# Optimization experiments

Measured on AMD Instinct MI355X. Metric: run time of the kernel, lower is better.

## Reference

```python
import jax, jax.numpy as jnp
import numpy as np

N_R, N_V, D, E_RR, L, G = 50000, 2000, 128, 800000, 3, 32


def setup_inputs() -> dict:
    key = jax.random.key(0)
    ks = jax.random.split(key, 10)
    x_real = jax.random.normal(ks[0], (N_R, D), dtype=jnp.float32)
    x_virtual = jax.random.normal(ks[1], (N_V, D), dtype=jnp.float32)
    # params: [num_layers, 3 relations (r_to_r, r_to_v, v_to_r), D, D]
    W_root = jax.random.normal(ks[2], (L, 3, D, D), dtype=jnp.float32) * 0.05
    W_nbr = jax.random.normal(ks[3], (L, 3, D, D), dtype=jnp.float32) * 0.05
    bias = jax.random.normal(ks[4], (L, 3, D), dtype=jnp.float32) * 0.05
    edge_rr = jax.random.randint(ks[5], (2, E_RR), 0, N_R)
    # one virtual-node edge per real node (hierarchical virtual nodes)
    src_rv = jnp.arange(N_R)
    dst_rv = jax.random.randint(ks[6], (N_R,), 0, N_V)
    edge_rv = jnp.stack([src_rv, dst_rv])          # real -> virtual
    edge_vr = jnp.stack([dst_rv, src_rv])          # virtual -> real
    batch_real = jnp.sort(jax.random.randint(ks[7], (N_R,), 0, G))
    return {
        "x_real": x_real, "x_virtual": x_virtual,
        "W_root": W_root, "W_nbr": W_nbr, "bias": bias,
        "edge_rr": edge_rr, "edge_rv": edge_rv, "edge_vr": edge_vr,
        "batch_real": batch_real,
    }


def _graph_conv(x_src, x_dst, src, dst, Wr, Wn, b, n_dst):
    # PyG GraphConv-style: root transform + sum-aggregated neighbor messages
    msg = jax.ops.segment_sum(x_src[src] @ Wn, dst, num_segments=n_dst)
    return x_dst @ Wr + msg + b


def _forward(x_real, x_virtual, W_root, W_nbr, bias, edge_rr, edge_rv, edge_vr, batch_real):
    x_r, x_v = x_real, x_virtual
    n_r, n_v = x_r.shape[0], x_v.shape[0]
    for l in range(W_root.shape[0]):
        # HeteroConv with aggr='sum': sum relation outputs per destination type
        c_rr = _graph_conv(x_r, x_r, edge_rr[0], edge_rr[1], W_root[l, 0], W_nbr[l, 0], bias[l, 0], n_r)
        c_vr = _graph_conv(x_v, x_r, edge_vr[0], edge_vr[1], W_root[l, 2], W_nbr[l, 2], bias[l, 2], n_r)
        c_rv = _graph_conv(x_r, x_v, edge_rv[0], edge_rv[1], W_root[l, 1], W_nbr[l, 1], bias[l, 1], n_v)
        # activation + dropout (eval mode -> identity)
        x_r = jax.nn.relu(c_rr + c_vr)
        x_v = jax.nn.relu(c_rv)
    # mean readout over real nodes per graph
    counts = jax.ops.segment_sum(jnp.ones((n_r,), x_r.dtype), batch_real, num_segments=G)
    graph_emb = jax.ops.segment_sum(x_r, batch_real, num_segments=G) / jnp.maximum(counts, 1.0)[:, None]
    return x_r, graph_emb


def reference(x_real, x_virtual, W_root, W_nbr, bias, edge_rr, edge_rv, edge_vr, batch_real):
    node_embedding, graph_embedding = _forward(
        x_real, x_virtual, W_root, W_nbr, bias, edge_rr, edge_rv, edge_vr, batch_real)
    return node_embedding, graph_embedding
```

## Files before the change

kernel.cpp:

```cpp
#include <hip/hip_runtime.h>
#include <hip/hip_bf16.h>

#define N_R   50000
#define N_V   2000
#define DIM   128
#define E_RR  800000
#define NLAY  3
#define NGR   32
#define RCHUNK 16

#define BUKD  128
#define NBUK  391
#define CHKE  2048
#define NCHK  391

typedef __attribute__((ext_vector_type(8))) short bf16x8;
typedef __attribute__((ext_vector_type(4))) float f32x4;
typedef __attribute__((ext_vector_type(2))) float f32x2;
typedef __attribute__((ext_vector_type(8))) unsigned char u8x8;

__device__ __forceinline__ ushort f2bf(float f) {
    unsigned u = __builtin_bit_cast(unsigned, f);
    unsigned r = (u + 0x7fffu + ((u >> 16) & 1u)) >> 16;
    return (ushort)r;
}
__device__ __forceinline__ float bf2f(ushort h) {
    unsigned u = ((unsigned)h) << 16;
    return __builtin_bit_cast(float, u);
}
__device__ __forceinline__ int lbound(const int* __restrict__ a, int n, int key) {
    int lo = 0, hi = n;
    while (lo < hi) { int mid = (lo + hi) >> 1; if (a[mid] < key) lo = mid + 1; else hi = mid; }
    return lo;
}

__device__ __forceinline__ void acc_u8row(
    unsigned w0, unsigned w1, float s,
    f32x2& a01, f32x2& a23, f32x2& a45, f32x2& a67)
{
    f32x2 sc = {s, s};
    a01 += sc * (f32x2){(float)(w0 & 0xffu), (float)((w0 >> 8) & 0xffu)};
    a23 += sc * (f32x2){(float)((w0 >> 16) & 0xffu), (float)(w0 >> 24)};
    a45 += sc * (f32x2){(float)(w1 & 0xffu), (float)((w1 >> 8) & 0xffu)};
    a67 += sc * (f32x2){(float)((w1 >> 16) & 0xffu), (float)(w1 >> 24)};
}

__global__ __launch_bounds__(256) void hist_kernel(
    const int* __restrict__ dst, int n, int* __restrict__ cnt)
{
    int i = blockIdx.x * 256 + threadIdx.x;
    if (i < n) atomicAdd(&cnt[dst[i]], 1);
}

__global__ __launch_bounds__(256) void scan_single_kernel(
    const int* __restrict__ cnt, int n, int nedges,
    int* __restrict__ rowptr, int* __restrict__ cursor)
{
    __shared__ int lds[256];
    __shared__ int carry;
    int t = threadIdx.x;
    if (t == 0) carry = 0;
    __syncthreads();
    for (int base = 0; base < n; base += 256) {
        int i = base + t;
        int v = (i < n) ? cnt[i] : 0;
        lds[t] = v;
        __syncthreads();
        #pragma unroll
        for (int off = 1; off < 256; off <<= 1) {
            int u = (t >= off) ? lds[t - off] : 0;
            __syncthreads();
            lds[t] += u;
            __syncthreads();
        }
        int excl = carry + lds[t] - v;
        if (i < n) {
            rowptr[i] = excl;
            if (cursor) cursor[i] = excl;
        }
        __syncthreads();
        if (t == 255) carry += lds[255];
        __syncthreads();
    }
    if (t == 0) rowptr[n] = nedges;
}

__global__ __launch_bounds__(256) void fill_kernel(
    const int* __restrict__ src, const int* __restrict__ dst, int n,
    int* __restrict__ cursor, int* __restrict__ col)
{
    int i = blockIdx.x * 256 + threadIdx.x;
    if (i < n) {
        int p = atomicAdd(&cursor[dst[i]], 1);
        col[p] = src[i];
    }
}

__global__ __launch_bounds__(256) void bkt_count_kernel(
    const int* __restrict__ dst, unsigned short* __restrict__ cnt2d)
{
    __shared__ int h[NBUK];
    int t = threadIdx.x, c = blockIdx.x;
    for (int i = t; i < NBUK; i += 256) h[i] = 0;
    __syncthreads();
    int e0 = c * CHKE, e1 = min(e0 + CHKE, E_RR);
    for (int e = e0 + t; e < e1; e += 256) atomicAdd(&h[dst[e] >> 7], 1);
    __syncthreads();
    for (int i = t; i < NBUK; i += 256)
        cnt2d[(size_t)c * NBUK + i] = (unsigned short)h[i];
}

__global__ __launch_bounds__(64) void bkt_prefix_kernel(
    const unsigned short* __restrict__ cnt2d,
    unsigned short* __restrict__ rel2d, int* __restrict__ tot)
{
    int b = blockIdx.x, lane = threadIdx.x;
    int base = 0;
    for (int c0 = 0; c0 < NCHK; c0 += 64) {
        int c = c0 + lane;
        int v = (c < NCHK) ? (int)cnt2d[(size_t)c * NBUK + b] : 0;
        int s = v;
        #pragma unroll
        for (int off = 1; off < 64; off <<= 1) {
            int u = __shfl_up(s, off);
            if (lane >= off) s += u;
        }
        if (c < NCHK) rel2d[(size_t)c * NBUK + b] = (unsigned short)(base + s - v);
        base += __shfl(s, 63);
    }
    if (lane == 0) tot[b] = base;
}

__global__ __launch_bounds__(256) void bkt_scatter_kernel(
    const int* __restrict__ src, const int* __restrict__ dst,
    const unsigned short* __restrict__ rel2d, const int* __restrict__ bstart,
    unsigned* __restrict__ ebuf)
{
    __shared__ int cur[NBUK];
    int t = threadIdx.x, c = blockIdx.x;
    for (int i = t; i < NBUK; i += 256)
        cur[i] = bstart[i] + (int)rel2d[(size_t)c * NBUK + i];
    __syncthreads();
    int e0 = c * CHKE, e1 = min(e0 + CHKE, E_RR);
    for (int e = e0 + t; e < e1; e += 256) {
        int d = dst[e];
        int p = atomicAdd(&cur[d >> 7], 1);
        ebuf[p] = ((unsigned)d << 16) | (unsigned)src[e];
    }
}

__global__ __launch_bounds__(256) void bkt_fine_kernel(
    const unsigned* __restrict__ ebuf, const int* __restrict__ bstart,
    int* __restrict__ rowptr, unsigned short* __restrict__ col16)
{
    __shared__ int cnt[BUKD];
    __shared__ int sc[BUKD];
    __shared__ int cur[BUKD];
    int b = blockIdx.x, t = threadIdx.x;
    int s0 = bstart[b], s1 = bstart[b + 1];
    if (t < BUKD) cnt[t] = 0;
    __syncthreads();
    for (int e = s0 + t; e < s1; e += 256)
        atomicAdd(&cnt[(ebuf[e] >> 16) & (BUKD - 1)], 1);
    __syncthreads();
    if (t < BUKD) sc[t] = cnt[t];
    __syncthreads();
    #pragma unroll
    for (int off = 1; off < BUKD; off <<= 1) {
        int v = (t < BUKD && t >= off) ? sc[t - off] : 0;
        __syncthreads();
        if (t < BUKD) sc[t] += v;
        __syncthreads();
    }
    if (t < BUKD) {
        int ex = sc[t] - cnt[t];
        int d = b * BUKD + t;
        if (d < N_R) rowptr[d] = s0 + ex;
        cur[t] = ex;
    }
    if (b == NBUK - 1 && t == 0) rowptr[N_R] = E_RR;
    __syncthreads();
    for (int e = s0 + t; e < s1; e += 256) {
        unsigned pk = ebuf[e];
        int p = atomicAdd(&cur[(pk >> 16) & (BUKD - 1)], 1);
        col16[s0 + p] = (unsigned short)(pk & 0xffffu);
    }
}

__global__ __launch_bounds__(256) void repack_kernel(
    const unsigned short* __restrict__ col16,
    const unsigned short* __restrict__ sbf,
    unsigned* __restrict__ colp)
{
    int i = blockIdx.x * 256 + threadIdx.x;
    if (i < E_RR) {
        unsigned c = col16[i];
        colp[i] = c | ((unsigned)sbf[c] << 16);
    }
}

__global__ __launch_bounds__(256) void quant_input_kernel(
    const float* __restrict__ in, unsigned char* __restrict__ q,
    unsigned short* __restrict__ sbf)
{
    int w = (blockIdx.x * 256 + threadIdx.x) >> 6;
    int lane = threadIdx.x & 63;
    if (w >= N_R) return;
    float2 v = *(const float2*)(in + (size_t)w * DIM + lane * 2);
    float mx = fmaxf(fabsf(v.x), fabsf(v.y));
    #pragma unroll
    for (int off = 1; off < 64; off <<= 1)
        mx = fmaxf(mx, __shfl_xor(mx, off));
    ushort sb = f2bf(mx / 127.f);
    float s = bf2f(sb);
    float inv = (s > 0.f) ? 1.f / s : 0.f;
    int q0 = min(255, max(0, __float2int_rn(v.x * inv) + 128));
    int q1 = min(255, max(0, __float2int_rn(v.y * inv) + 128));
    *(ushort*)(q + (size_t)w * DIM + lane * 2) = (ushort)(q0 | (q1 << 8));
    if (lane == 0) sbf[w] = sb;
}

__global__ __launch_bounds__(256) void build_wt_kernel(
    const float* __restrict__ Wroot, const float* __restrict__ Wnbr,
    ushort* __restrict__ WT)
{
    int idx = blockIdx.x * 256 + threadIdx.x;
    if (idx >= NLAY * DIM * 2 * DIM) return;
    int k = idx & 255;
    int n = (idx >> 8) & 127;
    int l = idx >> 15;
    float v;
    if (k < DIM) {
        const float* base = Wroot + (size_t)l * 3 * DIM * DIM;
        v = base[(size_t)k * DIM + n] + base[(size_t)(2 * DIM + k) * DIM + n];
    } else {
        v = Wnbr[((size_t)l * 3 * DIM + (k - DIM)) * DIM + n];
    }
    WT[idx] = f2bf(v);
}

__global__ __launch_bounds__(256) void combine_b_kernel(
    const float* __restrict__ bias, float* __restrict__ bc)
{
    int idx = blockIdx.x * 256 + threadIdx.x;
    if (idx >= NLAY * DIM) return;
    int l = idx / DIM;
    int rest = idx - l * DIM;
    const float* base = bias + (size_t)l * 3 * DIM;
    bc[idx] = base[rest] + base[2 * DIM + rest];
}

__global__ __launch_bounds__(256) void vlayer_kernel(
    const int* __restrict__ rowptr, const int* __restrict__ col,
    const unsigned char* __restrict__ Xq, const unsigned short* __restrict__ sbf,
    float zp, const float* __restrict__ xv,
    const float* __restrict__ Wn2, const float* __restrict__ Wr1,
    const float* __restrict__ Wn1, const float* __restrict__ b1,
    float* __restrict__ Tv, float* __restrict__ xv_next, int doNext)
{
    __shared__ float part[4 * DIM];
    __shared__ float arv_s[DIM];
    int v = blockIdx.x;
    int t = threadIdx.x;
    int wave = t >> 6, lane = t & 63;

    if (doNext) {
        int beg = rowptr[v], end = rowptr[v + 1];
        float a0 = 0.f, a1 = 0.f, ssum = 0.f;
        for (int e = beg + wave; e < end; e += 4) {
            int c = col[e];
            float s = bf2f(sbf[c]);
            uchar2 u = *(const uchar2*)(Xq + (size_t)c * DIM + lane * 2);
            a0 += s * (float)u.x;
            a1 += s * (float)u.y;
            ssum += s;
        }
        part[wave * DIM + lane * 2 + 0] = a0 - zp * ssum;
        part[wave * DIM + lane * 2 + 1] = a1 - zp * ssum;
        __syncthreads();
        if (t < DIM)
            arv_s[t] = part[t] + part[DIM + t] + part[2 * DIM + t] + part[3 * DIM + t];
        __syncthreads();
    }

    const float* arow = xv + (size_t)v * DIM;
    if (t < DIM) {
        float tacc = 0.f;
        #pragma unroll 8
        for (int k = 0; k < DIM; ++k)
            tacc += arow[k] * Wn2[(size_t)k * DIM + t];
        Tv[(size_t)v * DIM + t] = tacc;
    } else if (doNext) {
        int c = t - DIM;
        float nacc = 0.f;
        #pragma unroll 4
        for (int k = 0; k < DIM; ++k)
            nacc += arow[k] * Wr1[(size_t)k * DIM + c]
                  + arv_s[k] * Wn1[(size_t)k * DIM + c];
        xv_next[(size_t)v * DIM + c] = fmaxf(nacc + b1[c], 0.f);
    }
}

__global__ __launch_bounds__(256) void fused_layer_kernel(
    const int* __restrict__ rowptr, const unsigned* __restrict__ colp,
    const unsigned char* __restrict__ Xq, const unsigned short* __restrict__ sbf,
    float zp, const ushort* __restrict__ WT,
    const float* __restrict__ Tv,  const int* __restrict__ vmap,
    const float* __restrict__ bias,
    float* __restrict__ outF,
    unsigned char* __restrict__ Xq_out, unsigned short* __restrict__ sbf_out, int M)
{
    __shared__ ushort a2[16 * DIM];
    __shared__ float ost[16 * DIM];
    int t = threadIdx.x;

    int wave = t >> 6, lane = t & 63;
    int rlo = lane & 15, hi = lane >> 4;
    int row0 = blockIdx.x * 16;
    int arowc = min(row0 + rlo, M - 1);
    float sa = bf2f(sbf[arowc]);
    bf16x8 afr[8];
    #pragma unroll
    for (int j = 0; j < 4; ++j) {
        u8x8 uv = *(const u8x8*)(Xq + (size_t)arowc * DIM + 32 * j + 8 * hi);
        bf16x8 f;
        #pragma unroll
        for (int q = 0; q < 8; ++q)
            f[q] = (short)f2bf(sa * ((float)uv[q] - zp));
        afr[j] = f;
    }
    int vr[4];
    #pragma unroll
    for (int i = 0; i < 4; ++i)
        vr[i] = vmap[min(row0 + 4 * hi + i, M - 1)];

    {
        int g = t >> 3;
        int li = t & 7;
        int row = g >> 1;
        int half = g & 1;
        int drow = min(row0 + row, M - 1);
        int beg = rowptr[drow], end = rowptr[drow + 1];
        const unsigned char* XH = Xq + half * 64 + li * 8;
        f32x2 a01 = {0.f, 0.f}, a23 = {0.f, 0.f};
        f32x2 a45 = {0.f, 0.f}, a67 = {0.f, 0.f};
        float ssum = 0.f;
        int e = beg;
        for (; e + 3 < end; e += 4) {
            unsigned p0 = colp[e + 0], p1 = colp[e + 1];
            unsigned p2 = colp[e + 2], p3 = colp[e + 3];
            float s0 = bf2f((ushort)(p0 >> 16)), s1 = bf2f((ushort)(p1 >> 16));
            float s2 = bf2f((ushort)(p2 >> 16)), s3 = bf2f((ushort)(p3 >> 16));
            uint2 d0 = *(const uint2*)(XH + (size_t)(p0 & 0xffffu) * DIM);
            uint2 d1 = *(const uint2*)(XH + (size_t)(p1 & 0xffffu) * DIM);
            uint2 d2 = *(const uint2*)(XH + (size_t)(p2 & 0xffffu) * DIM);
            uint2 d3 = *(const uint2*)(XH + (size_t)(p3 & 0xffffu) * DIM);
            acc_u8row(d0.x, d0.y, s0, a01, a23, a45, a67);
            acc_u8row(d1.x, d1.y, s1, a01, a23, a45, a67);
            acc_u8row(d2.x, d2.y, s2, a01, a23, a45, a67);
            acc_u8row(d3.x, d3.y, s3, a01, a23, a45, a67);
            ssum += (s0 + s1) + (s2 + s3);
        }
        for (; e < end; ++e) {
            unsigned p0 = colp[e];
            float s0 = bf2f((ushort)(p0 >> 16));
            uint2 d0 = *(const uint2*)(XH + (size_t)(p0 & 0xffffu) * DIM);
            acc_u8row(d0.x, d0.y, s0, a01, a23, a45, a67);
            ssum += s0;
        }
        float zs = zp * ssum;
        bf16x8 pk;
        pk[0] = (short)f2bf(a01.x - zs);
        pk[1] = (short)f2bf(a01.y - zs);
        pk[2] = (short)f2bf(a23.x - zs);
        pk[3] = (short)f2bf(a23.y - zs);
        pk[4] = (short)f2bf(a45.x - zs);
        pk[5] = (short)f2bf(a45.y - zs);
        pk[6] = (short)f2bf(a67.x - zs);
        pk[7] = (short)f2bf(a67.y - zs);
        int byte = row * 256 + ((half * 128 + li * 16) ^ ((row & 7) << 4));
        *(bf16x8*)((char*)a2 + byte) = pk;
    }
    __syncthreads();

    #pragma unroll
    for (int jj = 0; jj < 4; ++jj) {
        int byte = rlo * 256 + ((64 * jj + 16 * hi) ^ ((rlo & 7) << 4));
        afr[4 + jj] = *(const bf16x8*)((const char*)a2 + byte);
    }

    f32x4 acc[2];
    #pragma unroll
    for (int n = 0; n < 2; ++n) acc[n] = (f32x4){0.f, 0.f, 0.f, 0.f};

    #pragma unroll
    for (int n = 0; n < 2; ++n) {
        int nt = wave * 2 + n;
        const ushort* wrow = WT + (size_t)(nt * 16 + rlo) * (2 * DIM);
        #pragma unroll
        for (int j = 0; j < 8; ++j) {
            bf16x8 bfr = *(const bf16x8*)(wrow + 32 * j + 8 * hi);
            acc[n] = __builtin_amdgcn_mfma_f32_16x16x32_bf16(afr[j], bfr, acc[n], 0, 0, 0);
        }
    }

    if (outF) {
        #pragma unroll
        for (int n = 0; n < 2; ++n) {
            int ncol = (wave * 2 + n) * 16 + rlo;
            float bv = bias[ncol];
            #pragma unroll
            for (int i = 0; i < 4; ++i) {
                int orow = row0 + 4 * hi + i;
                if (orow >= M) continue;
                float v = acc[n][i] + bv + Tv[(size_t)vr[i] * DIM + ncol];
                outF[(size_t)orow * DIM + ncol] = fmaxf(v, 0.f);
            }
        }
    } else {
        #pragma unroll
        for (int n = 0; n < 2; ++n) {
            int ncol = (wave * 2 + n) * 16 + rlo;
            float bv = bias[ncol];
            #pragma unroll
            for (int i = 0; i < 4; ++i) {
                float v = acc[n][i] + bv + Tv[(size_t)vr[i] * DIM + ncol];
                ost[(4 * hi + i) * DIM + ncol] = fmaxf(v, 0.f);
            }
        }
        __syncthreads();
        int g16 = t >> 4;
        int li16 = t & 15;
        int orow = row0 + g16;
        float4 f0 = *(const float4*)(ost + g16 * DIM + li16 * 8);
        float4 f1 = *(const float4*)(ost + g16 * DIM + li16 * 8 + 4);
        float mx = fmaxf(fmaxf(fmaxf(f0.x, f0.y), fmaxf(f0.z, f0.w)),
                         fmaxf(fmaxf(f1.x, f1.y), fmaxf(f1.z, f1.w)));
        #pragma unroll
        for (int off = 1; off < 16; off <<= 1)
            mx = fmaxf(mx, __shfl_xor(mx, off, 16));
        ushort sb = f2bf(mx / 255.f);
        float s = bf2f(sb);
        float inv = (s > 0.f) ? 1.f / s : 0.f;
        if (orow < M) {
            u8x8 qv;
            qv[0] = (unsigned char)min(255, __float2int_rn(f0.x * inv));
            qv[1] = (unsigned char)min(255, __float2int_rn(f0.y * inv));
            qv[2] = (unsigned char)min(255, __float2int_rn(f0.z * inv));
            qv[3] = (unsigned char)min(255, __float2int_rn(f0.w * inv));
            qv[4] = (unsigned char)min(255, __float2int_rn(f1.x * inv));
            qv[5] = (unsigned char)min(255, __float2int_rn(f1.y * inv));
            qv[6] = (unsigned char)min(255, __float2int_rn(f1.z * inv));
            qv[7] = (unsigned char)min(255, __float2int_rn(f1.w * inv));
            *(u8x8*)(Xq_out + (size_t)orow * DIM + li16 * 8) = qv;
            if (li16 == 0) sbf_out[orow] = sb;
        }
    }
}

__global__ __launch_bounds__(256) void readout_kernel(
    const float* __restrict__ xr, const int* __restrict__ batch,
    float* __restrict__ gsum, int nrows)
{
    __shared__ float lds[256 * 4];
    int g = blockIdx.x / RCHUNK;
    int chunk = blockIdx.x % RCHUNK;
    int lo = lbound(batch, nrows, g);
    int hi = lbound(batch, nrows, g + 1);
    int len = hi - lo;
    if (len == 0) return;
    int per = (len + RCHUNK - 1) / RCHUNK;
    int r0 = lo + chunk * per;
    int r1 = min(r0 + per, hi);

    int t = threadIdx.x;
    int c4 = (t & 31) << 2;
    int rsub = t >> 5;

    float4 acc = make_float4(0.f, 0.f, 0.f, 0.f);
    for (int r = r0 + rsub; r < r1; r += 8) {
        float4 v = *(const float4*)(xr + (size_t)r * DIM + c4);
        acc.x += v.x; acc.y += v.y; acc.z += v.z; acc.w += v.w;
    }
    *(float4*)(lds + t * 4) = acc;
    __syncthreads();
    if (rsub == 0) {
        float4 s = make_float4(0.f, 0.f, 0.f, 0.f);
        #pragma unroll
        for (int j = 0; j < 8; ++j) {
            float4 v = *(const float4*)(lds + (j * 32 + t) * 4);
            s.x += v.x; s.y += v.y; s.z += v.z; s.w += v.w;
        }
        atomicAdd(&gsum[(size_t)g * DIM + c4 + 0], s.x);
        atomicAdd(&gsum[(size_t)g * DIM + c4 + 1], s.y);
        atomicAdd(&gsum[(size_t)g * DIM + c4 + 2], s.z);
        atomicAdd(&gsum[(size_t)g * DIM + c4 + 3], s.w);
    }
}

__global__ __launch_bounds__(256) void finalize_kernel(
    const float* __restrict__ gsum, const int* __restrict__ batch,
    float* __restrict__ out, int nrows)
{
    int idx = blockIdx.x * 256 + threadIdx.x;
    if (idx >= NGR * DIM) return;
    int g = idx >> 7;
    int lo = lbound(batch, nrows, g);
    int hi = lbound(batch, nrows, g + 1);
    float c = fmaxf((float)(hi - lo), 1.f);
    out[idx] = gsum[idx] / c;
}

extern "C" void kernel_launch(void* const* d_in, const int* in_sizes, int n_in,
                              void* d_out, int out_size, void* d_ws, size_t ws_size,
                              hipStream_t stream)
{
    const float* x_real    = (const float*)d_in[0];
    const float* x_virtual = (const float*)d_in[1];
    const float* W_root    = (const float*)d_in[2];
    const float* W_nbr     = (const float*)d_in[3];
    const float* bias      = (const float*)d_in[4];
    const int*   edge_rr   = (const int*)d_in[5];
    const int*   edge_rv   = (const int*)d_in[6];
    const int*   edge_vr   = (const int*)d_in[7];
    const int*   batch     = (const int*)d_in[8];

    float* out = (float*)d_out;

    float*  ws    = (float*)d_ws;
    float*  Tv    = ws;
    float*  xv_a  = Tv   + (size_t)N_V * DIM;
    float*  xv_b  = xv_a + (size_t)N_V * DIM;
    float*  bc    = xv_b + (size_t)N_V * DIM;
    float*  gsum  = bc   + (size_t)NLAY * DIM;
    ushort* WT    = (ushort*)(gsum + NGR * DIM);
    int* iws       = (int*)(WT + (size_t)NLAY * DIM * 2 * DIM);
    int* rowptr_rr = iws;
    int* cnt_v     = rowptr_rr + N_R + 1;
    int* rowptr_rv = cnt_v + N_V;
    int* cursor_rv = rowptr_rv + N_V + 1;
    int* col_rv    = cursor_rv + N_V;
    int* tot       = col_rv + N_R;
    int* bstart    = tot + NBUK;
    unsigned* colp = (unsigned*)(bstart + NBUK + 1);
    unsigned* ebuf = colp + E_RR;
    unsigned short* col16 = (unsigned short*)(ebuf + E_RR);
    unsigned short* cnt2d = col16 + E_RR;
    unsigned short* rel2d = cnt2d + (size_t)NCHK * NBUK;
    unsigned short* sbf0  = rel2d + (size_t)NCHK * NBUK;
    unsigned short* sbf1  = sbf0 + N_R;
    unsigned short* sbf2  = sbf1 + N_R;
    unsigned char* Q0 = (unsigned char*)(sbf2 + N_R);
    unsigned char* Q1 = Q0 + (size_t)N_R * DIM;
    unsigned char* Q2 = Q1 + (size_t)N_R * DIM;

    const int* rr_src = edge_rr;
    const int* rr_dst = edge_rr + E_RR;
    const int* rv_src = edge_rv;
    const int* rv_dst = edge_rv + N_R;

    bkt_count_kernel<<<NCHK, 256, 0, stream>>>(rr_dst, cnt2d);
    bkt_prefix_kernel<<<NBUK, 64, 0, stream>>>(cnt2d, rel2d, tot);
    scan_single_kernel<<<1, 256, 0, stream>>>(tot, NBUK, E_RR, bstart, nullptr);
    bkt_scatter_kernel<<<NCHK, 256, 0, stream>>>(rr_src, rr_dst, rel2d, bstart, ebuf);
    bkt_fine_kernel<<<NBUK, 256, 0, stream>>>(ebuf, bstart, rowptr_rr, col16);

    hipMemsetAsync(cnt_v, 0, (size_t)N_V * sizeof(int), stream);
    hist_kernel<<<(N_R + 255) / 256, 256, 0, stream>>>(rv_dst, N_R, cnt_v);
    scan_single_kernel<<<1, 256, 0, stream>>>(cnt_v, N_V, N_R, rowptr_rv, cursor_rv);
    fill_kernel<<<(N_R + 255) / 256, 256, 0, stream>>>(rv_src, rv_dst, N_R, cursor_rv, col_rv);

    build_wt_kernel<<<(NLAY * DIM * 2 * DIM + 255) / 256, 256, 0, stream>>>(W_root, W_nbr, WT);
    combine_b_kernel<<<(NLAY * DIM + 255) / 256, 256, 0, stream>>>(bias, bc);
    quant_input_kernel<<<(N_R * 64 + 255) / 256, 256, 0, stream>>>(x_real, Q0, sbf0);

    unsigned char* Qcur = Q0;  unsigned short* Scur = sbf0;
    const float* cur_xv = x_virtual;

    for (int l = 0; l < NLAY; ++l) {
        const float* Wn1 = W_nbr + ((size_t)l * 3 + 1) * DIM * DIM;
        const float* Wn2 = W_nbr + ((size_t)l * 3 + 2) * DIM * DIM;
        const float* Wr1 = W_root + ((size_t)l * 3 + 1) * DIM * DIM;
        const float* b1  = bias + ((size_t)l * 3 + 1) * DIM;

        int doNext = (l < NLAY - 1);
        float zp = (l == 0) ? 128.f : 0.f;
        float* xv_out = (l & 1) ? xv_b : xv_a;

        repack_kernel<<<(E_RR + 255) / 256, 256, 0, stream>>>(col16, Scur, colp);

        vlayer_kernel<<<N_V, 256, 0, stream>>>(
            rowptr_rv, col_rv, Qcur, Scur, zp, cur_xv,
            Wn2, Wr1, Wn1, b1, Tv, xv_out, doNext);

        unsigned char*  Qnext = (l == 0) ? Q1 : Q2;
        unsigned short* Snext = (l == 0) ? sbf1 : sbf2;
        float* outF = (l == NLAY - 1) ? out : nullptr;
        fused_layer_kernel<<<(N_R + 15) / 16, 256, 0, stream>>>(
            rowptr_rr, colp, Qcur, Scur, zp, WT + (size_t)l * DIM * 2 * DIM,
            Tv, edge_vr, bc + (size_t)l * DIM,
            outF, outF ? nullptr : Qnext, outF ? nullptr : Snext, N_R);

        if (doNext) { cur_xv = xv_out; Qcur = Qnext; Scur = Snext; }
    }

    hipMemsetAsync(gsum, 0, (size_t)NGR * DIM * sizeof(float), stream);
    readout_kernel<<<NGR * RCHUNK, 256, 0, stream>>>(out, batch, gsum, N_R);
    finalize_kernel<<<(NGR * DIM + 255) / 256, 256, 0, stream>>>(
        gsum, batch, out + (size_t)N_R * DIM, N_R);
}
```

Baseline: 322.9 us.

## Pad CSR rows to multiples of four and fuse colp repack into vlayer

Splits the fine bucket sort into count and scatter passes so that each destination row's edge list is padded to a multiple of four with sentinel entries. The sentinels become zero-scale entries, which lets the gather loop use 128-bit colp loads and drop the scalar tail loop. The per-layer repack kernel is removed and its work is folded into the start of vlayer_kernel, saving three launches. The cost is extra padded edges to process, two extra preprocessing launches, and padded entries that still gather row 0. The colp uint4 loads depend on 16-byte alignment, which the new workspace ordering appears intended to provide.

```diff
diff --git a/kernel.cpp b/kernel.cpp
--- a/kernel.cpp
+++ b/kernel.cpp
@@ -5,6 +5,7 @@
 #define N_V   2000
 #define DIM   128
 #define E_RR  800000
+#define EPAD  (E_RR + 4 * N_R)
 #define NLAY  3
 #define NGR   32
 #define RCHUNK 16
@@ -82,7 +83,7 @@
         if (t == 255) carry += lds[255];
         __syncthreads();
     }
-    if (t == 0) rowptr[n] = nedges;
+    if (t == 0) rowptr[n] = (nedges >= 0) ? nedges : carry;
 }
 
 __global__ __launch_bounds__(256) void fill_kernel(
@@ -149,13 +150,12 @@
     }
 }
 
-__global__ __launch_bounds__(256) void bkt_fine_kernel(
+__global__ __launch_bounds__(256) void bkt_fineA_kernel(
     const unsigned* __restrict__ ebuf, const int* __restrict__ bstart,
-    int* __restrict__ rowptr, unsigned short* __restrict__ col16)
+    unsigned short* __restrict__ rowcnt, int* __restrict__ ptot)
 {
     __shared__ int cnt[BUKD];
-    __shared__ int sc[BUKD];
-    __shared__ int cur[BUKD];
+    __shared__ int red[BUKD];
     int b = blockIdx.x, t = threadIdx.x;
     int s0 = bstart[b], s1 = bstart[b + 1];
     if (t < BUKD) cnt[t] = 0;
@@ -163,7 +163,34 @@
     for (int e = s0 + t; e < s1; e += 256)
         atomicAdd(&cnt[(ebuf[e] >> 16) & (BUKD - 1)], 1);
     __syncthreads();
-    if (t < BUKD) sc[t] = cnt[t];
+    if (t < BUKD) {
+        rowcnt[(size_t)b * BUKD + t] = (unsigned short)cnt[t];
+        red[t] = (cnt[t] + 3) & ~3;
+    }
+    __syncthreads();
+    #pragma unroll
+    for (int off = 64; off > 0; off >>= 1) {
+        if (t < off) red[t] += red[t + off];
+        __syncthreads();
+    }
+    if (t == 0) ptot[b] = red[0];
+}
+
+__global__ __launch_bounds__(256) void bkt_fineB_kernel(
+    const unsigned* __restrict__ ebuf, const int* __restrict__ bstart,
+    const int* __restrict__ pbstart, const unsigned short* __restrict__ rowcnt,
+    int* __restrict__ rowptr, unsigned short* __restrict__ col16)
+{
+    __shared__ int sc[BUKD];
+    __shared__ int cur[BUKD];
+    __shared__ int fend[BUKD];
+    __shared__ int pend[BUKD];
+    int b = blockIdx.x, t = threadIdx.x;
+    int s0 = bstart[b], s1 = bstart[b + 1];
+    int p0 = pbstart[b];
+    int c = (t < BUKD) ? (int)rowcnt[(size_t)b * BUKD + t] : 0;
+    int pc = (c + 3) & ~3;
+    if (t < BUKD) sc[t] = pc;
     __syncthreads();
     #pragma unroll
     for (int off = 1; off < BUKD; off <<= 1) {
@@ -173,29 +200,24 @@
         __syncthreads();
     }
     if (t < BUKD) {
-        int ex = sc[t] - cnt[t];
+        int ex = sc[t] - pc;
         int d = b * BUKD + t;
-        if (d < N_R) rowptr[d] = s0 + ex;
+        if (d < N_R) rowptr[d] = p0 + ex;
         cur[t] = ex;
-    }
-    if (b == NBUK - 1 && t == 0) rowptr[N_R] = E_RR;
+        fend[t] = ex + c;
+        pend[t] = ex + pc;
+    }
+    if (b == NBUK - 1 && t == 0) rowptr[N_R] = pbstart[NBUK];
     __syncthreads();
     for (int e = s0 + t; e < s1; e += 256) {
         unsigned pk = ebuf[e];
         int p = atomicAdd(&cur[(pk >> 16) & (BUKD - 1)], 1);
-        col16[s0 + p] = (unsigned short)(pk & 0xffffu);
-    }
-}
-
-__global__ __launch_bounds__(256) void repack_kernel(
-    const unsigned short* __restrict__ col16,
-    const unsigned short* __restrict__ sbf,
-    unsigned* __restrict__ colp)
-{
-    int i = blockIdx.x * 256 + threadIdx.x;
-    if (i < E_RR) {
-        unsigned c = col16[i];
-        colp[i] = c | ((unsigned)sbf[c] << 16);
+        col16[p0 + p] = (unsigned short)(pk & 0xffffu);
+    }
+    __syncthreads();
+    if (t < BUKD) {
+        for (int p = fend[t]; p < pend[t]; ++p)
+            col16[p0 + p] = 0xFFFFu;
     }
 }
 
@@ -251,6 +273,8 @@
 }
 
 __global__ __launch_bounds__(256) void vlayer_kernel(
+    const int* __restrict__ rowptr_rr, const unsigned short* __restrict__ col16,
+    unsigned* __restrict__ colp,
     const int* __restrict__ rowptr, const int* __restrict__ col,
     const unsigned char* __restrict__ Xq, const unsigned short* __restrict__ sbf,
     float zp, const float* __restrict__ xv,
@@ -263,6 +287,14 @@
     int v = blockIdx.x;
     int t = threadIdx.x;
     int wave = t >> 6, lane = t & 63;
+
+    {
+        int ptot = rowptr_rr[N_R];
+        for (int i = v * 256 + t; i < ptot; i += N_V * 256) {
+            unsigned c = col16[i];
+            colp[i] = (c == 0xFFFFu) ? 0u : (c | ((unsigned)sbf[c] << 16));
+        }
+    }
 
     if (doNext) {
         int beg = rowptr[v], end = rowptr[v + 1];
@@ -345,28 +377,19 @@
         f32x2 a01 = {0.f, 0.f}, a23 = {0.f, 0.f};
         f32x2 a45 = {0.f, 0.f}, a67 = {0.f, 0.f};
         float ssum = 0.f;
-        int e = beg;
-        for (; e + 3 < end; e += 4) {
-            unsigned p0 = colp[e + 0], p1 = colp[e + 1];
-            unsigned p2 = colp[e + 2], p3 = colp[e + 3];
-            float s0 = bf2f((ushort)(p0 >> 16)), s1 = bf2f((ushort)(p1 >> 16));
-            float s2 = bf2f((ushort)(p2 >> 16)), s3 = bf2f((ushort)(p3 >> 16));
-            uint2 d0 = *(const uint2*)(XH + (size_t)(p0 & 0xffffu) * DIM);
-            uint2 d1 = *(const uint2*)(XH + (size_t)(p1 & 0xffffu) * DIM);
-            uint2 d2 = *(const uint2*)(XH + (size_t)(p2 & 0xffffu) * DIM);
-            uint2 d3 = *(const uint2*)(XH + (size_t)(p3 & 0xffffu) * DIM);
+        for (int e = beg; e < end; e += 4) {
+            uint4 p = *(const uint4*)(colp + e);
+            float s0 = bf2f((ushort)(p.x >> 16)), s1 = bf2f((ushort)(p.y >> 16));
+            float s2 = bf2f((ushort)(p.z >> 16)), s3 = bf2f((ushort)(p.w >> 16));
+            uint2 d0 = *(const uint2*)(XH + (size_t)(p.x & 0xffffu) * DIM);
+            uint2 d1 = *(const uint2*)(XH + (size_t)(p.y & 0xffffu) * DIM);
+            uint2 d2 = *(const uint2*)(XH + (size_t)(p.z & 0xffffu) * DIM);
+            uint2 d3 = *(const uint2*)(XH + (size_t)(p.w & 0xffffu) * DIM);
             acc_u8row(d0.x, d0.y, s0, a01, a23, a45, a67);
             acc_u8row(d1.x, d1.y, s1, a01, a23, a45, a67);
             acc_u8row(d2.x, d2.y, s2, a01, a23, a45, a67);
             acc_u8row(d3.x, d3.y, s3, a01, a23, a45, a67);
             ssum += (s0 + s1) + (s2 + s3);
-        }
-        for (; e < end; ++e) {
-            unsigned p0 = colp[e];
-            float s0 = bf2f((ushort)(p0 >> 16));
-            uint2 d0 = *(const uint2*)(XH + (size_t)(p0 & 0xffffu) * DIM);
-            acc_u8row(d0.x, d0.y, s0, a01, a23, a45, a67);
-            ssum += s0;
         }
         float zs = zp * ssum;
         bf16x8 pk;
@@ -534,7 +557,9 @@
     float*  bc    = xv_b + (size_t)N_V * DIM;
     float*  gsum  = bc   + (size_t)NLAY * DIM;
     ushort* WT    = (ushort*)(gsum + NGR * DIM);
-    int* iws       = (int*)(WT + (size_t)NLAY * DIM * 2 * DIM);
+    unsigned* colp = (unsigned*)(WT + (size_t)NLAY * DIM * 2 * DIM);
+    unsigned* ebuf = colp + EPAD;
+    int* iws       = (int*)(ebuf + E_RR);
     int* rowptr_rr = iws;
     int* cnt_v     = rowptr_rr + N_R + 1;
     int* rowptr_rv = cnt_v + N_V;
@@ -542,12 +567,13 @@
     int* col_rv    = cursor_rv + N_V;
     int* tot       = col_rv + N_R;
     int* bstart    = tot + NBUK;
-    unsigned* colp = (unsigned*)(bstart + NBUK + 1);
-    unsigned* ebuf = colp + E_RR;
-    unsigned short* col16 = (unsigned short*)(ebuf + E_RR);
-    unsigned short* cnt2d = col16 + E_RR;
+    int* ptot      = bstart + NBUK + 1;
+    int* pbstart   = ptot + NBUK;
+    unsigned short* col16 = (unsigned short*)(pbstart + NBUK + 1);
+    unsigned short* cnt2d = col16 + EPAD;
     unsigned short* rel2d = cnt2d + (size_t)NCHK * NBUK;
-    unsigned short* sbf0  = rel2d + (size_t)NCHK * NBUK;
+    unsigned short* rowcnt = rel2d + (size_t)NCHK * NBUK;
+    unsigned short* sbf0  = rowcnt + (size_t)NBUK * BUKD;
     unsigned short* sbf1  = sbf0 + N_R;
     unsigned short* sbf2  = sbf1 + N_R;
     unsigned char* Q0 = (unsigned char*)(sbf2 + N_R);
@@ -563,7 +589,10 @@
     bkt_prefix_kernel<<<NBUK, 64, 0, stream>>>(cnt2d, rel2d, tot);
     scan_single_kernel<<<1, 256, 0, stream>>>(tot, NBUK, E_RR, bstart, nullptr);
     bkt_scatter_kernel<<<NCHK, 256, 0, stream>>>(rr_src, rr_dst, rel2d, bstart, ebuf);
-    bkt_fine_kernel<<<NBUK, 256, 0, stream>>>(ebuf, bstart, rowptr_rr, col16);
+    bkt_fineA_kernel<<<NBUK, 256, 0, stream>>>(ebuf, bstart, rowcnt, ptot);
+    scan_single_kernel<<<1, 256, 0, stream>>>(ptot, NBUK, -1, pbstart, nullptr);
+    bkt_fineB_kernel<<<NBUK, 256, 0, stream>>>(ebuf, bstart, pbstart, rowcnt,
+                                               rowptr_rr, col16);
 
     hipMemsetAsync(cnt_v, 0, (size_t)N_V * sizeof(int), stream);
     hist_kernel<<<(N_R + 255) / 256, 256, 0, stream>>>(rv_dst, N_R, cnt_v);
@@ -587,9 +616,8 @@
         float zp = (l == 0) ? 128.f : 0.f;
         float* xv_out = (l & 1) ? xv_b : xv_a;
 
-        repack_kernel<<<(E_RR + 255) / 256, 256, 0, stream>>>(col16, Scur, colp);
-
         vlayer_kernel<<<N_V, 256, 0, stream>>>(
+            rowptr_rr, col16, colp,
             rowptr_rv, col_rv, Qcur, Scur, zp, cur_xv,
             Wn2, Wr1, Wn1, b1, Tv, xv_out, doNext);
 
```

New measurement: 317.4 us. Within noise of the previous version (-1.7%).
